# Performance work log

Hardware: AMD Instinct MI355X
Metric: run time of the kernel (lower is better)

The kernel has to match this reference:

```python
import jax, jax.numpy as jnp
import numpy as np

N, E, D, C, L, G = 50000, 1600000, 128, 10, 4, 512
BN_EPS = 1e-5


def setup_inputs() -> dict:
    key = jax.random.key(0)
    ks = jax.random.split(key, 16)
    s = 0.05  # weight init scale
    inp = {
        "x": jax.random.normal(ks[0], (N, D), dtype=jnp.float32),
        "edge_index": jax.random.randint(ks[1], (2, E), 0, N, dtype=jnp.int32),
        "batch": jnp.sort(jax.random.randint(ks[2], (N,), 0, G, dtype=jnp.int32)),
        "num_graphs": G,
        # GINConv inner MLP params (layer 0 input dim == D since num_features == num_hidden)
        "conv_W1": jax.random.normal(ks[3], (L, D, D), dtype=jnp.float32) * s,
        "conv_b1": jnp.zeros((L, D), dtype=jnp.float32),
        "conv_bn_g": jnp.ones((L, D), dtype=jnp.float32),
        "conv_bn_b": jnp.zeros((L, D), dtype=jnp.float32),
        "conv_W2": jax.random.normal(ks[4], (L, D, D), dtype=jnp.float32) * s,
        "conv_b2": jnp.zeros((L, D), dtype=jnp.float32),
        # outer BatchNorm after each conv
        "bn_g": jnp.ones((L, D), dtype=jnp.float32),
        "bn_b": jnp.zeros((L, D), dtype=jnp.float32),
        # per-scale classifier heads (L+1 of them; fcs[0] input dim == num_features == D)
        "fc_W": jax.random.normal(ks[5], (L + 1, D, C), dtype=jnp.float32) * s,
        "fc_b": jnp.zeros((L + 1, C), dtype=jnp.float32),
    }
    return inp


def _bn(h, g, b):
    # BatchNorm1d in training mode: batch stats over nodes, biased variance
    m = h.mean(axis=0)
    v = jnp.mean((h - m) ** 2, axis=0)
    return (h - m) * jax.lax.rsqrt(v + BN_EPS) * g + b


def reference(x, edge_index, batch, num_graphs, conv_W1, conv_b1, conv_bn_g,
              conv_bn_b, conv_W2, conv_b2, bn_g, bn_b, fc_W, fc_b):
    n_nodes = x.shape[0]
    src, dst = edge_index[0], edge_index[1]
    outs = [x]
    h = x
    for i in range(L):
        # GINConv (eps=0, aggr='add'): mlp(x + scatter_add of neighbor features)
        agg = jax.ops.segment_sum(h[src], dst, num_segments=n_nodes)  # [N, D]
        z = h + agg
        z = z @ conv_W1[i] + conv_b1[i]
        z = jax.nn.relu(_bn(z, conv_bn_g[i], conv_bn_b[i]))
        z = z @ conv_W2[i] + conv_b2[i]
        h = jax.nn.relu(_bn(z, bn_g[i], bn_b[i]))
        outs.append(h)
    out = None
    for i, o in enumerate(outs):
        pooled = jax.ops.segment_sum(o, batch, num_segments=num_graphs)  # [G, D]
        logits = pooled @ fc_W[i] + fc_b[i]
        out = logits if out is None else out + logits
    return jax.nn.log_softmax(out, axis=-1)
```

## Files before the change

### kernel.cpp

```cpp
#include <hip/hip_runtime.h>

#define NN 50000
#define EE 1600000
#define DD 128
#define CC 10
#define LLAY 4
#define GG 512
#define GD (GG*DD)
#define NB 196
#define BK_EDGES 6400
#define NSUB 16
#define SUBW 3125
#define WPAD 136

static constexpr float BN_EPS = 1e-5f;
static constexpr float INV_N = 1.0f / (float)NN;

typedef __bf16 bf16x8 __attribute__((ext_vector_type(8)));
typedef float f32x4 __attribute__((ext_vector_type(4)));

static __device__ __forceinline__ float bflo(unsigned u){ return __uint_as_float(u << 16); }
static __device__ __forceinline__ float bfhi(unsigned u){ return __uint_as_float(u & 0xffff0000u); }
static __device__ __forceinline__ unsigned short f2bf(float f){
    unsigned u = __float_as_uint(f);
    return (unsigned short)((u + 0x7fffu + ((u >> 16) & 1u)) >> 16);
}
static __device__ __forceinline__ unsigned packbf(float a, float b){
    return (unsigned)f2bf(a) | ((unsigned)f2bf(b) << 16);
}
static __device__ __forceinline__ bf16x8 ldfrag(const unsigned short* p){
    union { uint4 u; bf16x8 b; } t; t.u = *(const uint4*)p; return t.b;
}
static __device__ __forceinline__ bf16x8 asfrag(uint4 u){
    union { uint4 u; bf16x8 b; } t; t.u = u; return t.b;
}


__global__ void zero_k(int* p, int n){
    int i = blockIdx.x * 256 + threadIdx.x;
    if (i < n) p[i] = 0;
}

__global__ void convx_k(const float2* __restrict__ x2, unsigned* __restrict__ h32){
    int i = blockIdx.x * 256 + threadIdx.x;
    float2 v = x2[i];
    h32[i] = packbf(v.x, v.y);
}

__global__ void wprep_k(const float* __restrict__ W1, const float* __restrict__ W2,
                        unsigned short* __restrict__ Wtall){
    int idx = blockIdx.x * 256 + threadIdx.x;
    int mat = idx >> 14; int rr = idx & 16383;
    int k = rr >> 7; int j = rr & 127;
    const float* Wsrc = (mat < 4) ? (W1 + mat * 16384) : (W2 + (mat - 4) * 16384);
    Wtall[mat * 16384 + j * 128 + k] = f2bf(Wsrc[k * 128 + j]);
}

__global__ __launch_bounds__(256) void bhist_k(const int* __restrict__ dstA,
                                               int* __restrict__ bucketCnt){
    __shared__ int c[NB];
    int tid = threadIdx.x;
    if (tid < NB) c[tid] = 0;
    __syncthreads();
    int e0 = blockIdx.x * BK_EDGES;
    for (int i = tid; i < BK_EDGES; i += 256){
        int e = e0 + i;
        if (e < EE) atomicAdd(&c[dstA[e] >> 8], 1);
    }
    __syncthreads();
    if (tid < NB && c[tid] > 0) atomicAdd(&bucketCnt[tid], c[tid]);
}

__global__ __launch_bounds__(256) void bscan_k(const int* __restrict__ bucketCnt,
                                               int* __restrict__ bucketBase,
                                               int* __restrict__ bucketCur,
                                               int* __restrict__ rp){
    __shared__ int lds[256];
    int t = threadIdx.x;
    int v = (t < NB) ? bucketCnt[t] : 0;
    lds[t] = v; __syncthreads();
    for (int o = 1; o < 256; o <<= 1){
        int xv = 0; if (t >= o) xv = lds[t - o];
        __syncthreads(); lds[t] += xv; __syncthreads();
    }
    int excl = lds[t] - v;
    if (t < NB){ bucketBase[t] = excl; bucketCur[t] = excl; }
    if (t == 0){ bucketBase[NB] = EE; rp[NN] = EE; }
}

__global__ void gsearch_k(const int* __restrict__ batch, int* __restrict__ gstart){
    int g = blockIdx.x * 256 + threadIdx.x;
    if (g <= GG){
        int lo = 0, hi = NN;
        while (lo < hi){ int mid = (lo + hi) >> 1; if (batch[mid] < g) lo = mid + 1; else hi = mid; }
        gstart[g] = lo;
    }
}

__global__ __launch_bounds__(256) void binA_k(const int* __restrict__ srcA,
                                              const int* __restrict__ dstA,
                                              int* __restrict__ bucketCur,
                                              unsigned* __restrict__ binned){
    __shared__ int cnt[NB], bas[NB], off[NB];
    int tid = threadIdx.x;
    if (tid < NB){ cnt[tid] = 0; off[tid] = 0; }
    __syncthreads();
    int e0 = blockIdx.x * BK_EDGES;
    for (int i = tid; i < BK_EDGES; i += 256){
        int e = e0 + i;
        if (e < EE) atomicAdd(&cnt[dstA[e] >> 8], 1);
    }
    __syncthreads();
    if (tid < NB && cnt[tid] > 0) bas[tid] = atomicAdd(&bucketCur[tid], cnt[tid]);
    __syncthreads();
    for (int i = tid; i < BK_EDGES; i += 256){
        int e = e0 + i;
        if (e < EE){
            int d = dstA[e]; int b = d >> 8;
            int p = bas[b] + atomicAdd(&off[b], 1);
            binned[p] = (unsigned)srcA[e] | ((unsigned)(d & 255) << 17);
        }
    }
}

__global__ __launch_bounds__(256) void binB_k(const unsigned* __restrict__ binned,
                                              const int* __restrict__ bucketBase,
                                              int* __restrict__ rp,
                                              int* __restrict__ ssort){
    __shared__ int c16[256 * NSUB];
    __shared__ int b16[256 * NSUB];
    __shared__ int nt[256];
    int b = blockIdx.x, tid = threadIdx.x;
    int nb0 = b * 256;
    int nmax = NN - nb0; if (nmax > 256) nmax = 256;
    #pragma unroll
    for (int k = 0; k < NSUB; k++) c16[tid * NSUB + k] = 0;
    __syncthreads();
    int base = bucketBase[b];
    int end  = bucketBase[b + 1];
    for (int i = base + tid; i < end; i += 256){
        unsigned u = binned[i];
        int src = (int)(u & 0x1FFFFu); int dl = (int)(u >> 17);
        atomicAdd(&c16[dl * NSUB + src / SUBW], 1);
    }
    __syncthreads();
    int cc[NSUB]; int tot = 0;
    #pragma unroll
    for (int k = 0; k < NSUB; k++){ cc[k] = c16[tid * NSUB + k]; tot += cc[k]; }
    nt[tid] = tot; __syncthreads();
    for (int o = 1; o < 256; o <<= 1){
        int xv = 0; if (tid >= o) xv = nt[tid - o];
        __syncthreads(); nt[tid] += xv; __syncthreads();
    }
    int p = base + nt[tid] - tot;
    if (tid < nmax) rp[nb0 + tid] = p;
    int run = p;
    #pragma unroll
    for (int k = 0; k < NSUB; k++){ b16[tid * NSUB + k] = run; run += cc[k]; }
    #pragma unroll
    for (int k = 0; k < NSUB; k++) c16[tid * NSUB + k] = 0;
    __syncthreads();
    for (int i = base + tid; i < end; i += 256){
        unsigned u = binned[i];
        int src = (int)(u & 0x1FFFFu); int dl = (int)(u >> 17);
        int t = src / SUBW;
        int pos = b16[dl * NSUB + t] + atomicAdd(&c16[dl * NSUB + t], 1);
        ssort[pos] = src;
    }
}


__global__ __launch_bounds__(256) void agg_k(const unsigned* __restrict__ h32,
                                             const int* __restrict__ rp,
                                             const int* __restrict__ ssort,
                                             unsigned* __restrict__ z32,
                                             float* __restrict__ zstats){
    int tid = threadIdx.x;
    if (blockIdx.x == 0) zstats[tid] = 0.f;
    int n = blockIdx.x * 4 + (tid >> 6);
    int lane = tid & 63;
    unsigned self = h32[n * 64 + lane];
    float ax = bflo(self), ay = bfhi(self);
    int e  = __builtin_amdgcn_readfirstlane(rp[n]);
    int e1 = __builtin_amdgcn_readfirstlane(rp[n + 1]);
    for (; e + 7 < e1; e += 8){
        int s0 = ssort[e],     s1 = ssort[e + 1], s2 = ssort[e + 2], s3 = ssort[e + 3];
        int s4 = ssort[e + 4], s5 = ssort[e + 5], s6 = ssort[e + 6], s7 = ssort[e + 7];
        unsigned u0 = h32[s0 * 64 + lane];
        unsigned u1 = h32[s1 * 64 + lane];
        unsigned u2 = h32[s2 * 64 + lane];
        unsigned u3 = h32[s3 * 64 + lane];
        unsigned u4 = h32[s4 * 64 + lane];
        unsigned u5 = h32[s5 * 64 + lane];
        unsigned u6 = h32[s6 * 64 + lane];
        unsigned u7 = h32[s7 * 64 + lane];
        ax += bflo(u0) + bflo(u1); ay += bfhi(u0) + bfhi(u1);
        ax += bflo(u2) + bflo(u3); ay += bfhi(u2) + bfhi(u3);
        ax += bflo(u4) + bflo(u5); ay += bfhi(u4) + bfhi(u5);
        ax += bflo(u6) + bflo(u7); ay += bfhi(u6) + bfhi(u7);
    }
    for (; e < e1; ++e){
        unsigned u0 = h32[ssort[e] * 64 + lane];
        ax += bflo(u0); ay += bfhi(u0);
    }
    z32[n * 64 + lane] = packbf(ax, ay);
}

template<int TR>
__global__ __launch_bounds__(256) void gemm_k(const unsigned* __restrict__ A32,
                                              const unsigned short* __restrict__ Wtg,
                                              const float* __restrict__ bias,
                                              unsigned short* __restrict__ Cst,
                                              const float* __restrict__ stats,
                                              const float* __restrict__ gma,
                                              const float* __restrict__ bta,
                                              float* __restrict__ ostats,
                                              float* __restrict__ zstats){
    __shared__ __align__(16) unsigned short Wl[64 * WPAD];
    __shared__ float sred[512];
    __shared__ __align__(16) float sl[128], tl[128];
    int tid = threadIdx.x;
    int slice = blockIdx.x & 1;
    int tileb = blockIdx.x >> 1;
    if (blockIdx.x == 0 && zstats) zstats[tid] = 0.f;
    {
        const uint4* src = (const uint4*)(Wtg + slice * 64 * 128);
        uint4* dst = (uint4*)Wl;
        #pragma unroll
        for (int i = 0; i < 4; i++){
            int idx = tid + 256 * i;
            int row = idx >> 4, c16 = idx & 15;
            dst[row * (WPAD / 8) + c16] = src[idx];
        }
    }
    if (TR && tid < 128){
        float mean = stats[tid] * INV_N;
        float q    = stats[128 + tid] * INV_N;
        float inv  = rsqrtf(q - mean * mean + BN_EPS);
        float s    = gma[tid] * inv;
        sl[tid] = s; tl[tid] = bta[tid] - mean * s;
    }
    __syncthreads();

    int wv = tid >> 6, lane = tid & 63;
    int rowbase = tileb * 128 + wv * 32;
    int r0 = rowbase + (lane & 15);
    int r1 = r0 + 16;
    int kd = (lane >> 4) * 4;

    uint4 va[4], vb[4];
    #pragma unroll
    for (int ks = 0; ks < 4; ks++){
        va[ks] = (r0 < NN) ? *(const uint4*)(A32 + r0 * 64 + ks * 16 + kd) : make_uint4(0,0,0,0);
        vb[ks] = (r1 < NN) ? *(const uint4*)(A32 + r1 * 64 + ks * 16 + kd) : make_uint4(0,0,0,0);
    }
    if (TR){
        #pragma unroll
        for (int ks = 0; ks < 4; ks++){
            int q = ks * 8 + (lane >> 4) * 2;
            float4 sA = ((const float4*)sl)[q], sB = ((const float4*)sl)[q + 1];
            float4 tA = ((const float4*)tl)[q], tB = ((const float4*)tl)[q + 1];
            float fs[8] = {sA.x, sA.y, sA.z, sA.w, sB.x, sB.y, sB.z, sB.w};
            float ft[8] = {tA.x, tA.y, tA.z, tA.w, tB.x, tB.y, tB.z, tB.w};
            unsigned* pa = (unsigned*)&va[ks];
            unsigned* pb = (unsigned*)&vb[ks];
            #pragma unroll
            for (int c = 0; c < 4; c++){
                float f0 = fmaxf(bflo(pa[c]) * fs[2*c] + ft[2*c], 0.f);
                float f1 = fmaxf(bfhi(pa[c]) * fs[2*c+1] + ft[2*c+1], 0.f);
                pa[c] = packbf(f0, f1);
                f0 = fmaxf(bflo(pb[c]) * fs[2*c] + ft[2*c], 0.f);
                f1 = fmaxf(bfhi(pb[c]) * fs[2*c+1] + ft[2*c+1], 0.f);
                pb[c] = packbf(f0, f1);
            }
        }
    }

    f32x4 acc[2][4];
    #pragma unroll
    for (int a = 0; a < 2; a++)
        #pragma unroll
        for (int b = 0; b < 4; b++) acc[a][b] = (f32x4){0.f, 0.f, 0.f, 0.f};

    #pragma unroll
    for (int ks = 0; ks < 4; ks++){
        int wk = ks * 32 + (lane >> 4) * 8;
        bf16x8 a0 = asfrag(va[ks]);
        bf16x8 a1 = asfrag(vb[ks]);
        #pragma unroll
        for (int ct = 0; ct < 4; ++ct){
            bf16x8 b = ldfrag(&Wl[(ct * 16 + (lane & 15)) * WPAD + wk]);
            acc[0][ct] = __builtin_amdgcn_mfma_f32_16x16x32_bf16(a0, b, acc[0][ct], 0, 0, 0);
            acc[1][ct] = __builtin_amdgcn_mfma_f32_16x16x32_bf16(a1, b, acc[1][ct], 0, 0, 0);
        }
    }

    int cl = lane & 15, rq = lane >> 4;
    float colS[4], colQ[4];
    #pragma unroll
    for (int ct = 0; ct < 4; ++ct){
        int col = slice * 64 + ct * 16 + cl;
        float bv = bias[col];
        float ps = 0.f, pq = 0.f;
        #pragma unroll
        for (int rt = 0; rt < 2; ++rt){
            #pragma unroll
            for (int rr2 = 0; rr2 < 4; ++rr2){
                int grow = rowbase + rt * 16 + rq * 4 + rr2;
                if (grow < NN){
                    float val = acc[rt][ct][rr2] + bv;
                    Cst[grow * 128 + col] = f2bf(val);
                    ps += val; pq += val * val;
                }
            }
        }
        ps += __shfl_xor(ps, 16); pq += __shfl_xor(pq, 16);
        ps += __shfl_xor(ps, 32); pq += __shfl_xor(pq, 32);
        colS[ct] = ps; colQ[ct] = pq;
    }
    if (rq == 0){
        #pragma unroll
        for (int ct = 0; ct < 4; ++ct){
            sred[wv * 64 + ct * 16 + cl]       = colS[ct];
            sred[256 + wv * 64 + ct * 16 + cl] = colQ[ct];
        }
    }
    __syncthreads();
    if (tid < 64){
        float s1 = sred[tid] + sred[64 + tid] + sred[128 + tid] + sred[192 + tid];
        float s2 = sred[256 + tid] + sred[320 + tid] + sred[384 + tid] + sred[448 + tid];
        atomicAdd(&ostats[slice * 64 + tid], s1);
        atomicAdd(&ostats[128 + slice * 64 + tid], s2);
    }
}

__global__ __launch_bounds__(256) void ewpool_k(const unsigned* __restrict__ z32,
                                                const float* __restrict__ stats,
                                                const float* __restrict__ g,
                                                const float* __restrict__ b,
                                                const int* __restrict__ gstart,
                                                unsigned* __restrict__ h32,
                                                float* __restrict__ outp){
    __shared__ float sd[512];
    int gid = blockIdx.x; int tid = threadIdx.x;
    int c = tid & 63, rs = tid >> 6;
    int c2 = c * 2;
    float m0 = stats[c2] * INV_N,     q0 = stats[128 + c2] * INV_N;
    float inv0 = rsqrtf(q0 - m0 * m0 + BN_EPS);
    float s0 = g[c2] * inv0, t0 = b[c2] - m0 * s0;
    float m1 = stats[c2 + 1] * INV_N, q1 = stats[129 + c2] * INV_N;
    float inv1 = rsqrtf(q1 - m1 * m1 + BN_EPS);
    float s1 = g[c2 + 1] * inv1, t1 = b[c2 + 1] - m1 * s1;
    int s = gstart[gid], e = gstart[gid + 1];
    float a0 = 0.f, a1 = 0.f;
    int n = s + rs;
    for (; n + 12 < e; n += 16){
        unsigned u0 = z32[n * 64 + c];
        unsigned u1 = z32[(n + 4) * 64 + c];
        unsigned u2 = z32[(n + 8) * 64 + c];
        unsigned u3 = z32[(n + 12) * 64 + c];
        float f0, f1;
        f0 = fmaxf(bflo(u0) * s0 + t0, 0.f); f1 = fmaxf(bfhi(u0) * s1 + t1, 0.f);
        h32[n * 64 + c] = packbf(f0, f1); a0 += f0; a1 += f1;
        f0 = fmaxf(bflo(u1) * s0 + t0, 0.f); f1 = fmaxf(bfhi(u1) * s1 + t1, 0.f);
        h32[(n + 4) * 64 + c] = packbf(f0, f1); a0 += f0; a1 += f1;
        f0 = fmaxf(bflo(u2) * s0 + t0, 0.f); f1 = fmaxf(bfhi(u2) * s1 + t1, 0.f);
        h32[(n + 8) * 64 + c] = packbf(f0, f1); a0 += f0; a1 += f1;
        f0 = fmaxf(bflo(u3) * s0 + t0, 0.f); f1 = fmaxf(bfhi(u3) * s1 + t1, 0.f);
        h32[(n + 12) * 64 + c] = packbf(f0, f1); a0 += f0; a1 += f1;
    }
    for (; n < e; n += 4){
        unsigned u = z32[n * 64 + c];
        float f0 = fmaxf(bflo(u) * s0 + t0, 0.f);
        float f1 = fmaxf(bfhi(u) * s1 + t1, 0.f);
        h32[n * 64 + c] = packbf(f0, f1);
        a0 += f0; a1 += f1;
    }
    sd[tid] = a0; sd[256 + tid] = a1; __syncthreads();
    if (tid < 64){
        float r0 = 0.f, r1 = 0.f;
        #pragma unroll
        for (int k2 = 0; k2 < 4; k2++){ r0 += sd[tid + 64 * k2]; r1 += sd[256 + tid + 64 * k2]; }
        outp[gid * 128 + 2 * tid] = r0; outp[gid * 128 + 2 * tid + 1] = r1;
    }
}

__global__ __launch_bounds__(256) void poolx_k(const float* __restrict__ x,
                                               const int* __restrict__ gstart,
                                               float* __restrict__ outp){
    __shared__ float sd[256];
    int g = blockIdx.x; int tid = threadIdx.x; int c = tid & 127, rs = tid >> 7;
    int s = gstart[g], e = gstart[g + 1];
    float a = 0;
    int n = s + rs;
    for (; n + 6 < e; n += 8){
        float v0 = x[n * 128 + c], v1 = x[(n + 2) * 128 + c];
        float v2 = x[(n + 4) * 128 + c], v3 = x[(n + 6) * 128 + c];
        a += (v0 + v1) + (v2 + v3);
    }
    for (; n < e; n += 2) a += x[n * 128 + c];
    sd[tid] = a; __syncthreads();
    if (tid < 128) outp[g * 128 + tid] = sd[tid] + sd[tid + 128];
}

__global__ __launch_bounds__(64) void final_k(const float* __restrict__ pooled,
                                              const float* __restrict__ fcW,
                                              const float* __restrict__ fcb,
                                              float* __restrict__ out){
    int g = blockIdx.x, l = threadIdx.x;
    float p0[5], p1[5];
    #pragma unroll
    for (int i = 0; i < 5; i++){
        p0[i] = pooled[i * GD + g * 128 + l];
        p1[i] = pooled[i * GD + g * 128 + 64 + l];
    }
    float lg[10];
    #pragma unroll
    for (int c2 = 0; c2 < 10; c2++){
        float s = 0;
        #pragma unroll
        for (int i = 0; i < 5; i++){
            s += p0[i] * fcW[(i * 128 + l) * 10 + c2];
            s += p1[i] * fcW[(i * 128 + 64 + l) * 10 + c2];
        }
        #pragma unroll
        for (int off = 32; off >= 1; off >>= 1) s += __shfl_down(s, off);
        lg[c2] = s;
    }
    if (l == 0){
        #pragma unroll
        for (int c2 = 0; c2 < 10; c2++){
            float bs = 0;
            #pragma unroll
            for (int i = 0; i < 5; i++) bs += fcb[i * 10 + c2];
            lg[c2] += bs;
        }
        float mx = lg[0];
        #pragma unroll
        for (int c2 = 1; c2 < 10; c2++) mx = fmaxf(mx, lg[c2]);
        float se = 0;
        #pragma unroll
        for (int c2 = 0; c2 < 10; c2++) se += expf(lg[c2] - mx);
        float lse = mx + logf(se);
        #pragma unroll
        for (int c2 = 0; c2 < 10; c2++) out[g * 10 + c2] = lg[c2] - lse;
    }
}


extern "C" void kernel_launch(void* const* d_in, const int* in_sizes, int n_in,
                              void* d_out, int out_size, void* d_ws, size_t ws_size,
                              hipStream_t stream){
    (void)in_sizes; (void)n_in; (void)out_size; (void)ws_size;
    const float* x     = (const float*)d_in[0];
    const int*   ei    = (const int*)d_in[1];
    const int*   batch = (const int*)d_in[2];
    const float* cW1   = (const float*)d_in[4];
    const float* cb1   = (const float*)d_in[5];
    const float* cbng  = (const float*)d_in[6];
    const float* cbnb  = (const float*)d_in[7];
    const float* cW2   = (const float*)d_in[8];
    const float* cb2   = (const float*)d_in[9];
    const float* bng   = (const float*)d_in[10];
    const float* bnb   = (const float*)d_in[11];
    const float* fcW   = (const float*)d_in[12];
    const float* fcb   = (const float*)d_in[13];

    char* base = (char*)d_ws;
    size_t off = 0;
    auto alloc = [&](size_t bytes) -> void* {
        void* p = base + off;
        off = (off + bytes + 255) & ~(size_t)255;
        return p;
    };
    unsigned*       hB     = (unsigned*)alloc((size_t)NN * 64 * 4);
    unsigned*       zA     = (unsigned*)alloc((size_t)NN * 64 * 4);
    unsigned*       zB     = (unsigned*)alloc((size_t)NN * 64 * 4);
    unsigned short* Wtall  = (unsigned short*)alloc(8 * 16384 * 2);
    int*            ssort  = (int*)alloc((size_t)EE * 4);
    int*            rp     = (int*)alloc((NN + 1) * 4);
    int*            gstart = (int*)alloc((GG + 1) * 4);
    int*            bucketCnt  = (int*)alloc(NB * 4);
    int*            bucketBase = (int*)alloc((NB + 1) * 4);
    int*            bucketCur  = (int*)alloc(NB * 4);
    float*          pooled = (float*)alloc((size_t)5 * GD * 4);
    float*          stats1 = (float*)alloc(256 * 4);
    float*          stats2 = (float*)alloc(256 * 4);
    unsigned*       binned = (unsigned*)zB;

    zero_k<<<1, 256, 0, stream>>>(bucketCnt, NB);
    convx_k<<<NN * 64 / 256, 256, 0, stream>>>((const float2*)x, hB);
    wprep_k<<<512, 256, 0, stream>>>(cW1, cW2, Wtall);
    bhist_k<<<(EE + BK_EDGES - 1) / BK_EDGES, 256, 0, stream>>>(ei + EE, bucketCnt);
    bscan_k<<<1, 256, 0, stream>>>(bucketCnt, bucketBase, bucketCur, rp);
    gsearch_k<<<3, 256, 0, stream>>>(batch, gstart);
    binA_k<<<(EE + BK_EDGES - 1) / BK_EDGES, 256, 0, stream>>>(ei, ei + EE, bucketCur, binned);
    binB_k<<<NB, 256, 0, stream>>>(binned, bucketBase, rp, ssort);
    poolx_k<<<GG, 256, 0, stream>>>(x, gstart, pooled);

    const int gemmGrid = 2 * ((NN + 127) / 128);
    for (int i = 0; i < LLAY; i++){
        agg_k<<<NN / 4, 256, 0, stream>>>(hB, rp, ssort, zA, stats1);
        gemm_k<0><<<gemmGrid, 256, 0, stream>>>(zA, Wtall + i * 16384, cb1 + i * 128,
                                                (unsigned short*)zB,
                                                nullptr, nullptr, nullptr, stats1, stats2);
        gemm_k<1><<<gemmGrid, 256, 0, stream>>>(zB, Wtall + (4 + i) * 16384, cb2 + i * 128,
                                                (unsigned short*)zA,
                                                stats1, cbng + i * 128, cbnb + i * 128, stats2, nullptr);
        ewpool_k<<<GG, 256, 0, stream>>>(zA, stats2, bng + i * 128, bnb + i * 128,
                                         gstart, hB, pooled + (size_t)(i + 1) * GD);
    }
    final_k<<<GG, 64, 0, stream>>>(pooled, fcW, fcb, (float*)d_out);
}
```

Baseline: 571.2 us.

## Fuse input conversion with pooling, widen aggregation loads, split pooling across blocks

The separate bf16 conversion and input pooling kernels become one kernel that reads x once and accumulates pooled sums with atomics. The edge aggregation kernel now has each half-wave take alternate edges with 8-byte loads and combines the halves with a shuffle, giving more gathers in flight per wave. Element-wise pooling runs four blocks per graph with atomic accumulation, so the pooled buffers must be zeroed first, done in the initial zero kernel and in the second GEMM. This adds atomic traffic and depends on the pooled buffer sitting inside the zeroed range of the allocation.

```diff
diff --git a/kernel.cpp b/kernel.cpp
--- a/kernel.cpp
+++ b/kernel.cpp
@@ -41,12 +41,6 @@
     if (i < n) p[i] = 0;
 }
 
-__global__ void convx_k(const float2* __restrict__ x2, unsigned* __restrict__ h32){
-    int i = blockIdx.x * 256 + threadIdx.x;
-    float2 v = x2[i];
-    h32[i] = packbf(v.x, v.y);
-}
-
 __global__ void wprep_k(const float* __restrict__ W1, const float* __restrict__ W2,
                         unsigned short* __restrict__ Wtall){
     int idx = blockIdx.x * 256 + threadIdx.x;
@@ -169,6 +163,30 @@
     }
 }
 
+__global__ __launch_bounds__(256) void convxpool_k(const float2* __restrict__ x2,
+                                                   const int* __restrict__ gstart,
+                                                   unsigned* __restrict__ h32,
+                                                   float* __restrict__ outp){
+    __shared__ float sd[512];
+    int b = blockIdx.x; int gid = b >> 2, chunk = b & 3;
+    int tid = threadIdx.x; int c = tid & 63, rs = tid >> 6;
+    int s = gstart[gid], e = gstart[gid + 1];
+    float a0 = 0.f, a1 = 0.f;
+    for (int n = s + chunk * 4 + rs; n < e; n += 16){
+        float2 v = x2[n * 64 + c];
+        h32[n * 64 + c] = packbf(v.x, v.y);
+        a0 += v.x; a1 += v.y;
+    }
+    sd[tid] = a0; sd[256 + tid] = a1; __syncthreads();
+    if (tid < 64){
+        float r0 = 0.f, r1 = 0.f;
+        #pragma unroll
+        for (int k2 = 0; k2 < 4; k2++){ r0 += sd[tid + 64 * k2]; r1 += sd[256 + tid + 64 * k2]; }
+        atomicAdd(&outp[gid * 128 + 2 * tid], r0);
+        atomicAdd(&outp[gid * 128 + 2 * tid + 1], r1);
+    }
+}
+
 
 __global__ __launch_bounds__(256) void agg_k(const unsigned* __restrict__ h32,
                                              const int* __restrict__ rp,
@@ -179,31 +197,37 @@
     if (blockIdx.x == 0) zstats[tid] = 0.f;
     int n = blockIdx.x * 4 + (tid >> 6);
     int lane = tid & 63;
-    unsigned self = h32[n * 64 + lane];
-    float ax = bflo(self), ay = bfhi(self);
+    int half = lane >> 5, j = lane & 31;
+    const uint2* h2 = (const uint2*)h32;
+    float a0 = 0.f, a1 = 0.f, a2 = 0.f, a3 = 0.f;
+    if (half == 0){
+        uint2 sv = h2[n * 32 + j];
+        a0 = bflo(sv.x); a1 = bfhi(sv.x); a2 = bflo(sv.y); a3 = bfhi(sv.y);
+    }
     int e  = __builtin_amdgcn_readfirstlane(rp[n]);
     int e1 = __builtin_amdgcn_readfirstlane(rp[n + 1]);
     for (; e + 7 < e1; e += 8){
-        int s0 = ssort[e],     s1 = ssort[e + 1], s2 = ssort[e + 2], s3 = ssort[e + 3];
-        int s4 = ssort[e + 4], s5 = ssort[e + 5], s6 = ssort[e + 6], s7 = ssort[e + 7];
-        unsigned u0 = h32[s0 * 64 + lane];
-        unsigned u1 = h32[s1 * 64 + lane];
-        unsigned u2 = h32[s2 * 64 + lane];
-        unsigned u3 = h32[s3 * 64 + lane];
-        unsigned u4 = h32[s4 * 64 + lane];
-        unsigned u5 = h32[s5 * 64 + lane];
-        unsigned u6 = h32[s6 * 64 + lane];
-        unsigned u7 = h32[s7 * 64 + lane];
-        ax += bflo(u0) + bflo(u1); ay += bfhi(u0) + bfhi(u1);
-        ax += bflo(u2) + bflo(u3); ay += bfhi(u2) + bfhi(u3);
-        ax += bflo(u4) + bflo(u5); ay += bfhi(u4) + bfhi(u5);
-        ax += bflo(u6) + bflo(u7); ay += bfhi(u6) + bfhi(u7);
-    }
-    for (; e < e1; ++e){
-        unsigned u0 = h32[ssort[e] * 64 + lane];
-        ax += bflo(u0); ay += bfhi(u0);
-    }
-    z32[n * 64 + lane] = packbf(ax, ay);
+        int s0 = ssort[e + half],     s1 = ssort[e + 2 + half];
+        int s2 = ssort[e + 4 + half], s3 = ssort[e + 6 + half];
+        uint2 u0 = h2[s0 * 32 + j];
+        uint2 u1 = h2[s1 * 32 + j];
+        uint2 u2 = h2[s2 * 32 + j];
+        uint2 u3 = h2[s3 * 32 + j];
+        a0 += (bflo(u0.x) + bflo(u1.x)) + (bflo(u2.x) + bflo(u3.x));
+        a1 += (bfhi(u0.x) + bfhi(u1.x)) + (bfhi(u2.x) + bfhi(u3.x));
+        a2 += (bflo(u0.y) + bflo(u1.y)) + (bflo(u2.y) + bflo(u3.y));
+        a3 += (bfhi(u0.y) + bfhi(u1.y)) + (bfhi(u2.y) + bfhi(u3.y));
+    }
+    for (; e + half < e1; e += 2){
+        uint2 u = h2[ssort[e + half] * 32 + j];
+        a0 += bflo(u.x); a1 += bfhi(u.x); a2 += bflo(u.y); a3 += bfhi(u.y);
+    }
+    a0 += __shfl_xor(a0, 32); a1 += __shfl_xor(a1, 32);
+    a2 += __shfl_xor(a2, 32); a3 += __shfl_xor(a3, 32);
+    if (half == 0){
+        uint2 o; o.x = packbf(a0, a1); o.y = packbf(a2, a3);
+        ((uint2*)z32)[n * 32 + j] = o;
+    }
 }
 
 template<int TR>
@@ -215,7 +239,8 @@
                                               const float* __restrict__ gma,
                                               const float* __restrict__ bta,
                                               float* __restrict__ ostats,
-                                              float* __restrict__ zstats){
+                                              float* __restrict__ zstats,
+                                              float* __restrict__ zpool){
     __shared__ __align__(16) unsigned short Wl[64 * WPAD];
     __shared__ float sred[512];
     __shared__ __align__(16) float sl[128], tl[128];
@@ -223,6 +248,7 @@
     int slice = blockIdx.x & 1;
     int tileb = blockIdx.x >> 1;
     if (blockIdx.x == 0 && zstats) zstats[tid] = 0.f;
+    if (zpool && blockIdx.x < 256) zpool[blockIdx.x * 256 + tid] = 0.f;
     {
         const uint4* src = (const uint4*)(Wtg + slice * 64 * 128);
         uint4* dst = (uint4*)Wl;
@@ -342,7 +368,8 @@
                                                 unsigned* __restrict__ h32,
                                                 float* __restrict__ outp){
     __shared__ float sd[512];
-    int gid = blockIdx.x; int tid = threadIdx.x;
+    int blk = blockIdx.x; int gid = blk >> 2, chunk = blk & 3;
+    int tid = threadIdx.x;
     int c = tid & 63, rs = tid >> 6;
     int c2 = c * 2;
     float m0 = stats[c2] * INV_N,     q0 = stats[128 + c2] * INV_N;
@@ -353,23 +380,17 @@
     float s1 = g[c2 + 1] * inv1, t1 = b[c2 + 1] - m1 * s1;
     int s = gstart[gid], e = gstart[gid + 1];
     float a0 = 0.f, a1 = 0.f;
-    int n = s + rs;
-    for (; n + 12 < e; n += 16){
+    int n = s + chunk * 4 + rs;
+    for (; n + 16 < e; n += 32){
         unsigned u0 = z32[n * 64 + c];
-        unsigned u1 = z32[(n + 4) * 64 + c];
-        unsigned u2 = z32[(n + 8) * 64 + c];
-        unsigned u3 = z32[(n + 12) * 64 + c];
+        unsigned u1 = z32[(n + 16) * 64 + c];
         float f0, f1;
         f0 = fmaxf(bflo(u0) * s0 + t0, 0.f); f1 = fmaxf(bfhi(u0) * s1 + t1, 0.f);
         h32[n * 64 + c] = packbf(f0, f1); a0 += f0; a1 += f1;
         f0 = fmaxf(bflo(u1) * s0 + t0, 0.f); f1 = fmaxf(bfhi(u1) * s1 + t1, 0.f);
-        h32[(n + 4) * 64 + c] = packbf(f0, f1); a0 += f0; a1 += f1;
-        f0 = fmaxf(bflo(u2) * s0 + t0, 0.f); f1 = fmaxf(bfhi(u2) * s1 + t1, 0.f);
-        h32[(n + 8) * 64 + c] = packbf(f0, f1); a0 += f0; a1 += f1;
-        f0 = fmaxf(bflo(u3) * s0 + t0, 0.f); f1 = fmaxf(bfhi(u3) * s1 + t1, 0.f);
-        h32[(n + 12) * 64 + c] = packbf(f0, f1); a0 += f0; a1 += f1;
-    }
-    for (; n < e; n += 4){
+        h32[(n + 16) * 64 + c] = packbf(f0, f1); a0 += f0; a1 += f1;
+    }
+    for (; n < e; n += 16){
         unsigned u = z32[n * 64 + c];
         float f0 = fmaxf(bflo(u) * s0 + t0, 0.f);
         float f1 = fmaxf(bfhi(u) * s1 + t1, 0.f);
@@ -381,26 +402,9 @@
         float r0 = 0.f, r1 = 0.f;
         #pragma unroll
         for (int k2 = 0; k2 < 4; k2++){ r0 += sd[tid + 64 * k2]; r1 += sd[256 + tid + 64 * k2]; }
-        outp[gid * 128 + 2 * tid] = r0; outp[gid * 128 + 2 * tid + 1] = r1;
-    }
-}
-
-__global__ __launch_bounds__(256) void poolx_k(const float* __restrict__ x,
-                                               const int* __restrict__ gstart,
-                                               float* __restrict__ outp){
-    __shared__ float sd[256];
-    int g = blockIdx.x; int tid = threadIdx.x; int c = tid & 127, rs = tid >> 7;
-    int s = gstart[g], e = gstart[g + 1];
-    float a = 0;
-    int n = s + rs;
-    for (; n + 6 < e; n += 8){
-        float v0 = x[n * 128 + c], v1 = x[(n + 2) * 128 + c];
-        float v2 = x[(n + 4) * 128 + c], v3 = x[(n + 6) * 128 + c];
-        a += (v0 + v1) + (v2 + v3);
-    }
-    for (; n < e; n += 2) a += x[n * 128 + c];
-    sd[tid] = a; __syncthreads();
-    if (tid < 128) outp[g * 128 + tid] = sd[tid] + sd[tid + 128];
+        atomicAdd(&outp[gid * 128 + 2 * tid], r0);
+        atomicAdd(&outp[gid * 128 + 2 * tid + 1], r1);
+    }
 }
 
 __global__ __launch_bounds__(64) void final_k(const float* __restrict__ pooled,
@@ -488,27 +492,29 @@
     float*          stats2 = (float*)alloc(256 * 4);
     unsigned*       binned = (unsigned*)zB;
 
-    zero_k<<<1, 256, 0, stream>>>(bucketCnt, NB);
-    convx_k<<<NN * 64 / 256, 256, 0, stream>>>((const float2*)x, hB);
+    int zwords = (int)(((char*)(pooled + GD) - (char*)bucketCnt) / 4);
+
+    zero_k<<<(zwords + 255) / 256, 256, 0, stream>>>(bucketCnt, zwords);
     wprep_k<<<512, 256, 0, stream>>>(cW1, cW2, Wtall);
     bhist_k<<<(EE + BK_EDGES - 1) / BK_EDGES, 256, 0, stream>>>(ei + EE, bucketCnt);
     bscan_k<<<1, 256, 0, stream>>>(bucketCnt, bucketBase, bucketCur, rp);
     gsearch_k<<<3, 256, 0, stream>>>(batch, gstart);
     binA_k<<<(EE + BK_EDGES - 1) / BK_EDGES, 256, 0, stream>>>(ei, ei + EE, bucketCur, binned);
     binB_k<<<NB, 256, 0, stream>>>(binned, bucketBase, rp, ssort);
-    poolx_k<<<GG, 256, 0, stream>>>(x, gstart, pooled);
+    convxpool_k<<<4 * GG, 256, 0, stream>>>((const float2*)x, gstart, hB, pooled);
 
     const int gemmGrid = 2 * ((NN + 127) / 128);
     for (int i = 0; i < LLAY; i++){
         agg_k<<<NN / 4, 256, 0, stream>>>(hB, rp, ssort, zA, stats1);
         gemm_k<0><<<gemmGrid, 256, 0, stream>>>(zA, Wtall + i * 16384, cb1 + i * 128,
                                                 (unsigned short*)zB,
-                                                nullptr, nullptr, nullptr, stats1, stats2);
+                                                nullptr, nullptr, nullptr, stats1, stats2, nullptr);
         gemm_k<1><<<gemmGrid, 256, 0, stream>>>(zB, Wtall + (4 + i) * 16384, cb2 + i * 128,
                                                 (unsigned short*)zA,
-                                                stats1, cbng + i * 128, cbnb + i * 128, stats2, nullptr);
-        ewpool_k<<<GG, 256, 0, stream>>>(zA, stats2, bng + i * 128, bnb + i * 128,
-                                         gstart, hB, pooled + (size_t)(i + 1) * GD);
+                                                stats1, cbng + i * 128, cbnb + i * 128, stats2, nullptr,
+                                                pooled + (size_t)(i + 1) * GD);
+        ewpool_k<<<4 * GG, 256, 0, stream>>>(zA, stats2, bng + i * 128, bnb + i * 128,
+                                             gstart, hB, pooled + (size_t)(i + 1) * GD);
     }
     final_k<<<GG, 64, 0, stream>>>(pooled, fcW, fcb, (float*)d_out);
 }
```

Measured after the change: 578.0 us. About the same (+1.2%).
